# Kernel tuning notes

Hardware: AMD Instinct MI355X
Metric: run time of the kernel (lower is better)

Reference implementation:

```python
import jax, jax.numpy as jnp
import numpy as np

EPS = 1e-5


def setup_inputs() -> dict:
    key = jax.random.key(0)
    k1, k2, k3 = jax.random.split(key, 3)
    B, C, H, W = 32, 64, 32, 32
    N = 16  # out_planes: number of independent BatchNorm2d branches
    x = jax.random.normal(k1, (B, C, H, W), dtype=jnp.float32)
    # per-branch affine params (torch init is gamma=1, beta=0; randomize for testing)
    gamma = jax.random.uniform(k2, (N, C), dtype=jnp.float32, minval=0.5, maxval=1.5)
    beta = jax.random.normal(k3, (N, C), dtype=jnp.float32) * 0.1
    return {"x": x, "gamma": gamma, "beta": beta}


def reference(x, gamma, beta):
    # All N BatchNorm2d branches see the identical input, so the batch
    # mean/var reduction over (B, H, W) is computed ONCE and shared.
    mean = jnp.mean(x, axis=(0, 2, 3))                    # [C]
    var = jnp.mean((x - mean[None, :, None, None]) ** 2,  # biased var, as torch BN
                   axis=(0, 2, 3))                        # [C]
    inv = jax.lax.rsqrt(var + EPS)                        # [C]
    xhat = (x - mean[None, :, None, None]) * inv[None, :, None, None]  # [B,C,H,W]
    # Per-branch affine, then concat along channel dim -> [B, N*C, H, W]
    out = gamma[None, :, :, None, None] * xhat[:, None] + beta[None, :, :, None, None]
    B, N, C, H, W = out.shape
    return out.reshape(B, N * C, H, W)
```

## Files before the change

kernel.cpp:

```cpp
#include <hip/hip_runtime.h>

#define CH      64
#define BATCH   32
#define NBR     16
#define HW      1024
#define NPC     32768

__global__ void __launch_bounds__(256) bn_partial(const float* __restrict__ x,
                                                  float* __restrict__ partials) {
    const int c = blockIdx.x & 63;
    const int g = blockIdx.x >> 6;
    const int t = threadIdx.x;

    float s = 0.f, sq = 0.f;
#pragma unroll
    for (int bb = 0; bb < 4; ++bb) {
        const int batch = g * 4 + bb;
        const float4 v = ((const float4*)x)[(batch * CH + c) * 256 + t];
        s  += v.x + v.y + v.z + v.w;
        sq += v.x * v.x + v.y * v.y + v.z * v.z + v.w * v.w;
    }

#pragma unroll
    for (int off = 32; off > 0; off >>= 1) {
        s  += __shfl_down(s, off);
        sq += __shfl_down(sq, off);
    }
    __shared__ float ls[4], lq[4];
    const int wave = t >> 6, lane = t & 63;
    if (lane == 0) { ls[wave] = s; lq[wave] = sq; }
    __syncthreads();
    if (t == 0) {
        const float S = ls[0] + ls[1] + ls[2] + ls[3];
        const float Q = lq[0] + lq[1] + lq[2] + lq[3];
        partials[(g * CH + c) * 2 + 0] = S;
        partials[(g * CH + c) * 2 + 1] = Q;
    }
}

__global__ void __launch_bounds__(1024) bn_finalize(const float* __restrict__ partials,
                                                    const float* __restrict__ gamma,
                                                    const float* __restrict__ beta,
                                                    float* __restrict__ scale,
                                                    float* __restrict__ shift) {
    const int t = threadIdx.x;
    const int c = t & 63;
    float S = 0.f, Q = 0.f;
#pragma unroll
    for (int g = 0; g < 8; ++g) {
        S += partials[(g * CH + c) * 2 + 0];
        Q += partials[(g * CH + c) * 2 + 1];
    }
    const float mean = S * (1.0f / NPC);
    const float var  = Q * (1.0f / NPC) - mean * mean;
    const float inv  = rsqrtf(var + 1e-5f);
    const float a    = gamma[t] * inv;
    scale[t] = a;
    shift[t] = beta[t] - a * mean;
}

__global__ void __launch_bounds__(256) bn_apply(const float* __restrict__ x,
                                                const float* __restrict__ scale,
                                                const float* __restrict__ shift,
                                                float* __restrict__ out) {
    const int idx = blockIdx.x * 256 + threadIdx.x;
    const int b   = idx >> 14;
    const int c   = (idx >> 8) & 63;
    const int hw4 = idx & 255;

    const float4 v = ((const float4*)x)[idx];
    float4* o4 = (float4*)out;

#pragma unroll
    for (int n = 0; n < NBR; ++n) {
        const float a = scale[n * CH + c];
        const float s = shift[n * CH + c];
        float4 o;
        o.x = a * v.x + s;
        o.y = a * v.y + s;
        o.z = a * v.z + s;
        o.w = a * v.w + s;
        o4[((b * 1024 + n * CH + c) << 8) + hw4] = o;
    }
}

extern "C" void kernel_launch(void* const* d_in, const int* in_sizes, int n_in,
                              void* d_out, int out_size, void* d_ws, size_t ws_size,
                              hipStream_t stream) {
    const float* x     = (const float*)d_in[0];
    const float* gamma = (const float*)d_in[1];
    const float* beta  = (const float*)d_in[2];
    float* out = (float*)d_out;
    float* ws  = (float*)d_ws;

    float* partials = ws;
    float* scale    = ws + 1024;
    float* shift    = ws + 2048;

    bn_partial <<<512, 256, 0, stream>>>(x, partials);
    bn_finalize<<<1, 1024, 0, stream>>>(partials, gamma, beta, scale, shift);
    bn_apply   <<<2048, 256, 0, stream>>>(x, scale, shift, out);
}
```

Before: 145.4 us.

## Fuse BN finalize into apply kernel and use nontemporal output stores

Removes the single-block finalize kernel and its launch. Each apply block now reduces the 8 partials for its channel itself and computes scale and shift inline from gamma and beta. Output writes use nontemporal stores so the large 128MB output stream does not pollute the cache. The cost is redundant partial reads per block, which are tiny and should hit in cache.

```diff
diff --git a/kernel.cpp b/kernel.cpp
--- a/kernel.cpp
+++ b/kernel.cpp
@@ -5,6 +5,8 @@
 #define NBR     16
 #define HW      1024
 #define NPC     32768
+
+typedef float vfloat4 __attribute__((ext_vector_type(4)));
 
 __global__ void __launch_bounds__(256) bn_partial(const float* __restrict__ x,
                                                   float* __restrict__ partials) {
@@ -16,7 +18,7 @@
 #pragma unroll
     for (int bb = 0; bb < 4; ++bb) {
         const int batch = g * 4 + bb;
-        const float4 v = ((const float4*)x)[(batch * CH + c) * 256 + t];
+        const vfloat4 v = ((const vfloat4*)x)[(batch * CH + c) * 256 + t];
         s  += v.x + v.y + v.z + v.w;
         sq += v.x * v.x + v.y * v.y + v.z * v.z + v.w * v.w;
     }
@@ -31,20 +33,20 @@
     if (lane == 0) { ls[wave] = s; lq[wave] = sq; }
     __syncthreads();
     if (t == 0) {
-        const float S = ls[0] + ls[1] + ls[2] + ls[3];
-        const float Q = lq[0] + lq[1] + lq[2] + lq[3];
-        partials[(g * CH + c) * 2 + 0] = S;
-        partials[(g * CH + c) * 2 + 1] = Q;
+        partials[(g * CH + c) * 2 + 0] = ls[0] + ls[1] + ls[2] + ls[3];
+        partials[(g * CH + c) * 2 + 1] = lq[0] + lq[1] + lq[2] + lq[3];
     }
 }
 
-__global__ void __launch_bounds__(1024) bn_finalize(const float* __restrict__ partials,
-                                                    const float* __restrict__ gamma,
-                                                    const float* __restrict__ beta,
-                                                    float* __restrict__ scale,
-                                                    float* __restrict__ shift) {
+__global__ void __launch_bounds__(256) bn_apply(const float* __restrict__ x,
+                                                const float* __restrict__ partials,
+                                                const float* __restrict__ gamma,
+                                                const float* __restrict__ beta,
+                                                float* __restrict__ out) {
+    const int c = blockIdx.x & 63;
+    const int b = blockIdx.x >> 6;
     const int t = threadIdx.x;
-    const int c = t & 63;
+
     float S = 0.f, Q = 0.f;
 #pragma unroll
     for (int g = 0; g < 8; ++g) {
@@ -52,35 +54,21 @@
         Q += partials[(g * CH + c) * 2 + 1];
     }
     const float mean = S * (1.0f / NPC);
-    const float var  = Q * (1.0f / NPC) - mean * mean;
-    const float inv  = rsqrtf(var + 1e-5f);
-    const float a    = gamma[t] * inv;
-    scale[t] = a;
-    shift[t] = beta[t] - a * mean;
-}
+    const float inv  = rsqrtf(Q * (1.0f / NPC) - mean * mean + 1e-5f);
 
-__global__ void __launch_bounds__(256) bn_apply(const float* __restrict__ x,
-                                                const float* __restrict__ scale,
-                                                const float* __restrict__ shift,
-                                                float* __restrict__ out) {
-    const int idx = blockIdx.x * 256 + threadIdx.x;
-    const int b   = idx >> 14;
-    const int c   = (idx >> 8) & 63;
-    const int hw4 = idx & 255;
-
-    const float4 v = ((const float4*)x)[idx];
-    float4* o4 = (float4*)out;
+    const vfloat4 v = ((const vfloat4*)x)[(b * CH + c) * 256 + t];
+    vfloat4* o4 = (vfloat4*)out;
 
 #pragma unroll
     for (int n = 0; n < NBR; ++n) {
-        const float a = scale[n * CH + c];
-        const float s = shift[n * CH + c];
-        float4 o;
+        const float a = gamma[n * CH + c] * inv;
+        const float s = beta[n * CH + c] - a * mean;
+        vfloat4 o;
         o.x = a * v.x + s;
         o.y = a * v.y + s;
         o.z = a * v.z + s;
         o.w = a * v.w + s;
-        o4[((b * 1024 + n * CH + c) << 8) + hw4] = o;
+        __builtin_nontemporal_store(o, &o4[((b * 1024 + n * CH + c) << 8) + t]);
     }
 }
 
@@ -91,13 +79,8 @@
     const float* gamma = (const float*)d_in[1];
     const float* beta  = (const float*)d_in[2];
     float* out = (float*)d_out;
-    float* ws  = (float*)d_ws;
+    float* partials = (float*)d_ws;
 
-    float* partials = ws;
-    float* scale    = ws + 1024;
-    float* shift    = ws + 2048;
-
-    bn_partial <<<512, 256, 0, stream>>>(x, partials);
-    bn_finalize<<<1, 1024, 0, stream>>>(partials, gamma, beta, scale, shift);
-    bn_apply   <<<2048, 256, 0, stream>>>(x, scale, shift, out);
+    bn_partial<<<512,  256, 0, stream>>>(x, partials);
+    bn_apply  <<<2048, 256, 0, stream>>>(x, partials, gamma, beta, out);
 }
```

Result: slower. 151.2 us (+4.0%).
